# Kernel tuning notes

Measured on AMD Instinct MI355X. Metric: run time of the kernel, lower is better.

## Reference

```python
import jax, jax.numpy as jnp
import numpy as np

D_MODEL = 1024
NUM_HEADS = 16
DEPTH = D_MODEL // NUM_HEADS


def setup_inputs() -> dict:
    key = jax.random.key(0)
    ks = jax.random.split(key, 11)
    B, S = 2, 2048
    s = 1.0 / np.sqrt(D_MODEL)
    return {
        "q": jax.random.normal(ks[0], (B, S, D_MODEL), jnp.float32),
        "k": jax.random.normal(ks[1], (B, S, D_MODEL), jnp.float32),
        "v": jax.random.normal(ks[2], (B, S, D_MODEL), jnp.float32),
        "wq": jax.random.normal(ks[3], (D_MODEL, D_MODEL), jnp.float32) * s,
        "bq": jax.random.normal(ks[4], (D_MODEL,), jnp.float32) * s,
        "wk": jax.random.normal(ks[5], (D_MODEL, D_MODEL), jnp.float32) * s,
        "bk": jax.random.normal(ks[6], (D_MODEL,), jnp.float32) * s,
        "wv": jax.random.normal(ks[7], (D_MODEL, D_MODEL), jnp.float32) * s,
        "bv": jax.random.normal(ks[8], (D_MODEL,), jnp.float32) * s,
        "wo": jax.random.normal(ks[9], (D_MODEL, D_MODEL), jnp.float32) * s,
        "bo": jax.random.normal(ks[10], (D_MODEL,), jnp.float32) * s,
    }


def _split_heads(x, B):
    # [B, S, D] -> [B, H, S, depth]
    return x.reshape(B, -1, NUM_HEADS, DEPTH).transpose(0, 2, 1, 3)


def reference(q, k, v, wq, bq, wk, bk, wv, bv, wo, bo):
    B, S, _ = q.shape
    # torch Linear: y = x @ W.T + b
    qh = _split_heads(q @ wq.T + bq, B)
    kh = _split_heads(k @ wk.T + bk, B)
    vh = _split_heads(v @ wv.T + bv, B)
    scale = jnp.sqrt(jnp.asarray(DEPTH, jnp.float32))
    scores = jnp.einsum("bhqd,bhkd->bhqk", qh, kh) / scale  # [B,H,S,S]
    attn = jax.nn.softmax(scores, axis=-1)
    out = jnp.einsum("bhqk,bhkd->bhqd", attn, vh)
    out = out.transpose(0, 2, 1, 3).reshape(B, S, D_MODEL)
    return out @ wo.T + bo
```

## Files before the change

### kernel.cpp

```cpp
#include <hip/hip_runtime.h>
#include <hip/hip_bf16.h>
#include <math.h>

#define D_MODEL 1024
#define NUM_HEADS 16
#define DEPTH 64
#define BATCH 2
#define SEQ 2048
#define N_TOK (BATCH * SEQ)

typedef short bf16x8 __attribute__((ext_vector_type(8)));
typedef _Float16 f16x8 __attribute__((ext_vector_type(8)));
typedef float f32x4  __attribute__((ext_vector_type(4)));
typedef unsigned short u16x8 __attribute__((ext_vector_type(8)));
typedef unsigned short u16x4 __attribute__((ext_vector_type(4)));
typedef unsigned int u32x4 __attribute__((ext_vector_type(4)));

__device__ __forceinline__ unsigned short f2b(float x) {
    return __builtin_bit_cast(unsigned short, __float2bfloat16(x));
}
__device__ __forceinline__ float b2f(unsigned short h) {
    return __builtin_bit_cast(float, (unsigned int)h << 16);
}
__device__ __forceinline__ unsigned short f2h(float x) {
    return __builtin_bit_cast(unsigned short, (_Float16)x);
}

__device__ __forceinline__ void pl32_swap(unsigned int& x, unsigned int& y) {
    auto r = __builtin_amdgcn_permlane32_swap(x, y, false, false);
    x = (unsigned int)r[0]; y = (unsigned int)r[1];
}
__device__ __forceinline__ void pl16_swap(unsigned int& x, unsigned int& y) {
    auto r = __builtin_amdgcn_permlane16_swap(x, y, false, false);
    x = (unsigned int)r[0]; y = (unsigned int)r[1];
}

__global__ __launch_bounds__(256) void prep_weights(
    const float* __restrict__ s0, const float* __restrict__ s1,
    const float* __restrict__ s2, const float* __restrict__ s3,
    unsigned short* __restrict__ f0, unsigned short* __restrict__ f1,
    unsigned short* __restrict__ f2,
    unsigned short* __restrict__ h3, unsigned short* __restrict__ l3,
    int n8)
{
    const int i = blockIdx.x * 256 + threadIdx.x;
    if (i >= n8) return;
    const int which = blockIdx.y;
    const float* src = (which == 0) ? s0 : (which == 1) ? s1 : (which == 2) ? s2 : s3;
    const float4 a0 = ((const float4*)src)[2 * i];
    const float4 a1 = ((const float4*)src)[2 * i + 1];
    const float xs[8] = {a0.x, a0.y, a0.z, a0.w, a1.x, a1.y, a1.z, a1.w};
    if (which < 3) {
        unsigned short* dst = (which == 0) ? f0 : (which == 1) ? f1 : f2;
        u16x8 o;
        #pragma unroll
        for (int e = 0; e < 8; ++e) o[e] = f2h(xs[e]);
        *(u16x8*)&dst[(size_t)i * 8] = o;
    } else {
        u16x8 h8, l8;
        #pragma unroll
        for (int e = 0; e < 8; ++e) {
            const unsigned short h = f2b(xs[e]);
            h8[e] = h;
            l8[e] = f2b(xs[e] - b2f(h));
        }
        *(u16x8*)&h3[(size_t)i * 8] = h8;
        *(u16x8*)&l3[(size_t)i * 8] = l8;
    }
}

__global__ __launch_bounds__(256, 3) void qkv_gemm(
    const float* __restrict__ Aq, const float* __restrict__ Ak,
    const float* __restrict__ Av,
    const unsigned short* __restrict__ Wq, const unsigned short* __restrict__ Wk,
    const unsigned short* __restrict__ Wv,
    const float* __restrict__ bq, const float* __restrict__ bk,
    const float* __restrict__ bv,
    void* __restrict__ Yq, void* __restrict__ Yk, void* __restrict__ Yvp)
{
    __shared__ unsigned short sA[128][64];
    __shared__ unsigned short sB[2][128][64];

    const int flat = (blockIdx.z * 32 + blockIdx.y) * 8 + blockIdx.x;
    const int swz  = (flat & 7) * 96 + (flat >> 3);
    const int bx = swz & 7;
    const int by = (swz >> 3) & 31;
    const int bz = swz >> 8;

    const float* Af = (bz == 0) ? Aq : (bz == 1) ? Ak : Av;
    const unsigned short* Bf = (bz == 0) ? Wq : (bz == 1) ? Wk : Wv;
    const float* bias = (bz == 0) ? bq : (bz == 1) ? bk : bv;
    const float scale = (bz == 0) ? 0.125f : 1.0f;
    const int mode = (bz == 2) ? 2 : 1;
    void* Yv = (bz == 0) ? Yq : (bz == 1) ? Yk : Yvp;

    const int tid  = threadIdx.x;
    const int wave = tid >> 6;
    const int lane = tid & 63;
    const int quad = lane >> 4;
    const int l16  = lane & 15;
    const int wm   = wave >> 1;
    const int wn   = wave & 1;

    const int j0 = bx * 128;
    const int i0 = by * 128;

    const int sc  = tid & 7;
    const int r32 = tid >> 3;

    f32x4 acc[4][4] = {};

    float4 fq[4][2];

    auto loadA = [&](int s) {
        const int k0 = s * 64;
        #pragma unroll
        for (int p = 0; p < 4; ++p) {
            const int row = p * 32 + r32;
            const int cg = (sc ^ (row & 7)) * 8;
            const float* srcp = &Af[(size_t)(i0 + row) * 1024 + k0 + cg];
            fq[p][0] = *(const float4*)srcp;
            fq[p][1] = *(const float4*)(srcp + 4);
        }
    };
    auto writeA = [&]() {
        #pragma unroll
        for (int p = 0; p < 4; ++p) {
            const int row = p * 32 + r32;
            const float xs[8] = {fq[p][0].x, fq[p][0].y, fq[p][0].z, fq[p][0].w,
                                 fq[p][1].x, fq[p][1].y, fq[p][1].z, fq[p][1].w};
            u16x8 o;
            #pragma unroll
            for (int e = 0; e < 8; ++e) o[e] = f2h(xs[e]);
            *(u16x8*)&sA[row][sc * 8] = o;
        }
    };
    auto stageB = [&](int buf, int s) {
        const int k0 = s * 64;
        #pragma unroll
        for (int p = 0; p < 4; ++p) {
            const int row = p * 32 + r32;
            const int cg = (sc ^ (row & 7)) * 8;
            __builtin_amdgcn_global_load_lds(
                (const __attribute__((address_space(1))) unsigned int*)
                    &Bf[(size_t)(j0 + row) * 1024 + k0 + cg],
                (__attribute__((address_space(3))) unsigned int*)&sB[buf][row][sc * 8],
                16, 0, 0);
        }
    };

    loadA(0);
    stageB(0, 0);
    writeA();
    __asm__ volatile("s_waitcnt vmcnt(0)" ::: "memory");
    __syncthreads();

    int cur = 0;
    for (int s = 0; s < 16; ++s) {
        if (s + 1 < 16) { loadA(s + 1); stageB(cur ^ 1, s + 1); }

        #pragma unroll
        for (int ks = 0; ks < 2; ++ks) {
            f16x8 a[4], b[4];
            #pragma unroll
            for (int mt = 0; mt < 4; ++mt) {
                const int row = wm * 64 + mt * 16 + l16;
                const int c = (((ks * 4 + quad) ^ (row & 7))) * 8;
                a[mt] = *(const f16x8*)&sA[row][c];
            }
            #pragma unroll
            for (int nt = 0; nt < 4; ++nt) {
                const int row = wn * 64 + nt * 16 + l16;
                const int c = (((ks * 4 + quad) ^ (row & 7))) * 8;
                b[nt] = *(const f16x8*)&sB[cur][row][c];
            }
            #pragma unroll
            for (int mt = 0; mt < 4; ++mt)
                #pragma unroll
                for (int nt = 0; nt < 4; ++nt)
                    acc[mt][nt] = __builtin_amdgcn_mfma_f32_16x16x32_f16(a[mt], b[nt], acc[mt][nt], 0, 0, 0);
        }

        __syncthreads();
        if (s + 1 < 16) {
            writeA();
            __asm__ volatile("s_waitcnt vmcnt(0)" ::: "memory");
        }
        __syncthreads();
        cur ^= 1;
    }

    float bvv[4];
    #pragma unroll
    for (int nt = 0; nt < 4; ++nt)
        bvv[nt] = bias[j0 + wn * 64 + nt * 16 + l16];

    #pragma unroll
    for (int mt = 0; mt < 4; ++mt) {
        const int ibase = i0 + wm * 64 + mt * 16 + quad * 4;
        #pragma unroll
        for (int nt = 0; nt < 4; ++nt) {
            const int j = j0 + wn * 64 + nt * 16 + l16;
            const int h = j >> 6, d = j & 63;
            if (mode == 1) {
                __hip_bfloat16* Y = (__hip_bfloat16*)Yv;
                #pragma unroll
                for (int r = 0; r < 4; ++r) {
                    const int i = ibase + r;
                    const int b = i >> 11, ss = i & (SEQ - 1);
                    Y[(((size_t)(b * NUM_HEADS + h) * SEQ) + ss) * DEPTH + d] =
                        __float2bfloat16((acc[mt][nt][r] + bvv[nt]) * scale);
                }
            } else {
                unsigned short* Y = (unsigned short*)Yv;
                const int b = ibase >> 11;
                u16x4 pack;
                #pragma unroll
                for (int r = 0; r < 4; ++r)
                    pack[r] = f2b((acc[mt][nt][r] + bvv[nt]) * scale);
                *(u16x4*)&Y[(((size_t)(b * NUM_HEADS + h) * DEPTH) + d) * SEQ
                            + (ibase & (SEQ - 1))] = pack;
            }
        }
    }
}

__global__ __launch_bounds__(512, 2) void gemm_bf16x3(
    const unsigned short* __restrict__ Ahi,
    const unsigned short* __restrict__ Alo,
    const unsigned short* __restrict__ Bhi,
    const unsigned short* __restrict__ Blo,
    const float* __restrict__ bias,
    float* __restrict__ Y,
    float scale)
{
    __shared__ unsigned short sAh[128][64];
    __shared__ unsigned short sAl[128][64];
    __shared__ unsigned short sBh[128][64];
    __shared__ unsigned short sBl[128][64];

    const int tid  = threadIdx.x;
    const int wave = tid >> 6;
    const int lane = tid & 63;
    const int quad = lane >> 4;
    const int l16  = lane & 15;
    const int wm   = wave >> 1;
    const int wn   = wave & 1;

    const int j0 = blockIdx.x * 128;
    const int i0 = blockIdx.y * 128;

    const int sc  = tid & 7;
    const int r64 = tid >> 3;

    u16x8 preH[4], preL[4];

    #pragma unroll
    for (int p = 0; p < 4; ++p) {
        const int row256 = p * 64 + r64;
        const bool isA = row256 < 128;
        const int row = isA ? row256 : row256 - 128;
        const unsigned short* srcH = isA ? Ahi : Bhi;
        const unsigned short* srcL = isA ? Alo : Blo;
        const int grow = (isA ? i0 : j0) + row;
        const int cg = (sc ^ (row & 7)) * 8;
        const size_t go = (size_t)grow * 1024 + cg;
        preH[p] = *(const u16x8*)&srcH[go];
        preL[p] = *(const u16x8*)&srcL[go];
    }

    f32x4 acc[2][4] = {};

    for (int s = 0; s < 16; ++s) {
        __syncthreads();

        #pragma unroll
        for (int p = 0; p < 4; ++p) {
            const int row256 = p * 64 + r64;
            const bool isA = row256 < 128;
            const int row = isA ? row256 : row256 - 128;
            unsigned short (*dh)[64] = isA ? sAh : sBh;
            unsigned short (*dl)[64] = isA ? sAl : sBl;
            *(u16x8*)&dh[row][sc * 8] = preH[p];
            *(u16x8*)&dl[row][sc * 8] = preL[p];
        }
        __syncthreads();

        if (s + 1 < 16) {
            const int k0 = (s + 1) * 64;
            #pragma unroll
            for (int p = 0; p < 4; ++p) {
                const int row256 = p * 64 + r64;
                const bool isA = row256 < 128;
                const int row = isA ? row256 : row256 - 128;
                const unsigned short* srcH = isA ? Ahi : Bhi;
                const unsigned short* srcL = isA ? Alo : Blo;
                const int grow = (isA ? i0 : j0) + row;
                const int cg = (sc ^ (row & 7)) * 8;
                const size_t go = (size_t)grow * 1024 + k0 + cg;
                preH[p] = *(const u16x8*)&srcH[go];
                preL[p] = *(const u16x8*)&srcL[go];
            }
        }

        #pragma unroll
        for (int ks = 0; ks < 2; ++ks) {
            bf16x8 ah[2], al[2], bh[4], bl[4];
            #pragma unroll
            for (int mt = 0; mt < 2; ++mt) {
                const int row = wm * 32 + mt * 16 + l16;
                const int c = (((ks * 4 + quad) ^ (row & 7))) * 8;
                ah[mt] = *(const bf16x8*)&sAh[row][c];
                al[mt] = *(const bf16x8*)&sAl[row][c];
            }
            #pragma unroll
            for (int nt = 0; nt < 4; ++nt) {
                const int row = wn * 64 + nt * 16 + l16;
                const int c = (((ks * 4 + quad) ^ (row & 7))) * 8;
                bh[nt] = *(const bf16x8*)&sBh[row][c];
                bl[nt] = *(const bf16x8*)&sBl[row][c];
            }
            #pragma unroll
            for (int mt = 0; mt < 2; ++mt)
                #pragma unroll
                for (int nt = 0; nt < 4; ++nt) {
                    acc[mt][nt] = __builtin_amdgcn_mfma_f32_16x16x32_bf16(ah[mt], bh[nt], acc[mt][nt], 0, 0, 0);
                    acc[mt][nt] = __builtin_amdgcn_mfma_f32_16x16x32_bf16(ah[mt], bl[nt], acc[mt][nt], 0, 0, 0);
                    acc[mt][nt] = __builtin_amdgcn_mfma_f32_16x16x32_bf16(al[mt], bh[nt], acc[mt][nt], 0, 0, 0);
                }
        }
    }

    float bv[4];
    #pragma unroll
    for (int nt = 0; nt < 4; ++nt)
        bv[nt] = bias[j0 + wn * 64 + nt * 16 + l16];

    #pragma unroll
    for (int mt = 0; mt < 2; ++mt) {
        const int ibase = i0 + wm * 32 + mt * 16 + quad * 4;
        #pragma unroll
        for (int nt = 0; nt < 4; ++nt) {
            const int j = j0 + wn * 64 + nt * 16 + l16;
            #pragma unroll
            for (int r = 0; r < 4; ++r)
                Y[(size_t)(ibase + r) * 1024 + j] = (acc[mt][nt][r] + bv[nt]) * scale;
        }
    }
}

__global__ __launch_bounds__(256) void flash_attn_mfma(
    const __hip_bfloat16* __restrict__ Qg,
    const __hip_bfloat16* __restrict__ Kg,
    const __hip_bfloat16* __restrict__ Vg,
    unsigned short* __restrict__ OHi,
    unsigned short* __restrict__ OLo)
{
    __shared__ unsigned short Ks[64][72];
    __shared__ unsigned short Vt[64][72];

    const int tid  = threadIdx.x;
    const int wave = tid >> 6;
    const int lane = tid & 63;
    const int quad = lane >> 4;
    const int l16  = lane & 15;

    const int bh = blockIdx.x >> 5;
    const int q0 = (blockIdx.x & 31) * 64;

    const unsigned short* Qu = (const unsigned short*)Qg + (size_t)bh * SEQ * DEPTH;
    const unsigned short* Ku = (const unsigned short*)Kg + (size_t)bh * SEQ * DEPTH;
    const unsigned short* Vu = (const unsigned short*)Vg + (size_t)bh * DEPTH * SEQ;

    const int qrow = q0 + wave * 16 + l16;
    bf16x8 qf[2];
    qf[0] = *(const bf16x8*)&Qu[(size_t)qrow * DEPTH + quad * 8];
    qf[1] = *(const bf16x8*)&Qu[(size_t)qrow * DEPTH + 32 + quad * 8];

    bf16x8 ones;
    #pragma unroll
    for (int e = 0; e < 8; ++e) ones[e] = (short)0x3F80;

    f32x4 o_acc[4] = {};
    f32x4 l_acc = {0.f, 0.f, 0.f, 0.f};

    const int srow = tid >> 3;
    const int sc8  = (tid & 7) * 8;
    u16x8 kpre[2], vpre[2];
    #pragma unroll
    for (int it = 0; it < 2; ++it) {
        const int row = it * 32 + srow;
        kpre[it] = *(const u16x8*)&Ku[(size_t)row * DEPTH + sc8];
        vpre[it] = *(const u16x8*)&Vu[(size_t)row * SEQ + sc8];
    }

    for (int t = 0; t < 32; ++t) {
        __syncthreads();

        #pragma unroll
        for (int it = 0; it < 2; ++it) {
            const int row = it * 32 + srow;
            *(u16x8*)&Ks[row][sc8] = kpre[it];
            *(u16x8*)&Vt[row][sc8] = vpre[it];
        }
        __syncthreads();

        if (t + 1 < 32) {
            const int k0 = (t + 1) * 64;
            #pragma unroll
            for (int it = 0; it < 2; ++it) {
                const int row = it * 32 + srow;
                kpre[it] = *(const u16x8*)&Ku[(size_t)(k0 + row) * DEPTH + sc8];
                vpre[it] = *(const u16x8*)&Vu[(size_t)row * SEQ + k0 + sc8];
            }
        }

        f32x4 s[4];
        #pragma unroll
        for (int nt = 0; nt < 4; ++nt) {
            s[nt] = f32x4{0.f, 0.f, 0.f, 0.f};
            bf16x8 kf0 = *(const bf16x8*)&Ks[nt * 16 + l16][quad * 8];
            s[nt] = __builtin_amdgcn_mfma_f32_16x16x32_bf16(kf0, qf[0], s[nt], 0, 0, 0);
            bf16x8 kf1 = *(const bf16x8*)&Ks[nt * 16 + l16][32 + quad * 8];
            s[nt] = __builtin_amdgcn_mfma_f32_16x16x32_bf16(kf1, qf[1], s[nt], 0, 0, 0);
        }

        unsigned int Wp[4][2];
        #pragma unroll
        for (int nt = 0; nt < 4; ++nt) {
            #pragma unroll
            for (int b = 0; b < 2; ++b) {
                const unsigned int lo = f2b(__expf(s[nt][2 * b]));
                const unsigned int hi = f2b(__expf(s[nt][2 * b + 1]));
                Wp[nt][b] = lo | (hi << 16);
            }
        }

        unsigned int pw[8];
        #pragma unroll
        for (int b = 0; b < 2; ++b) {
            unsigned int x = Wp[0][b], y = Wp[1][b];
            pl32_swap(x, y);
            pl16_swap(x, y);
            pw[b] = x; pw[2 + b] = y;
            x = Wp[2][b]; y = Wp[3][b];
            pl32_swap(x, y);
            pl16_swap(x, y);
            pw[4 + b] = x; pw[6 + b] = y;
        }
        bf16x8 pf[2];
        {
            u32x4 t0, t1;
            #pragma unroll
            for (int j = 0; j < 4; ++j) { t0[j] = pw[j]; t1[j] = pw[4 + j]; }
            pf[0] = __builtin_bit_cast(bf16x8, t0);
            pf[1] = __builtin_bit_cast(bf16x8, t1);
        }

        #pragma unroll
        for (int nt = 0; nt < 4; ++nt) {
            bf16x8 vf0 = *(const bf16x8*)&Vt[nt * 16 + l16][quad * 8];
            o_acc[nt] = __builtin_amdgcn_mfma_f32_16x16x32_bf16(pf[0], vf0, o_acc[nt], 0, 0, 0);
            bf16x8 vf1 = *(const bf16x8*)&Vt[nt * 16 + l16][32 + quad * 8];
            o_acc[nt] = __builtin_amdgcn_mfma_f32_16x16x32_bf16(pf[1], vf1, o_acc[nt], 0, 0, 0);
        }
        l_acc = __builtin_amdgcn_mfma_f32_16x16x32_bf16(pf[0], ones, l_acc, 0, 0, 0);
        l_acc = __builtin_amdgcn_mfma_f32_16x16x32_bf16(pf[1], ones, l_acc, 0, 0, 0);
    }

    const int b = bh / NUM_HEADS;
    const int h = bh % NUM_HEADS;
    #pragma unroll
    for (int r = 0; r < 4; ++r) {
        const float inv = 1.f / l_acc[r];
        const int row = q0 + wave * 16 + quad * 4 + r;
        #pragma unroll
        for (int nt = 0; nt < 4; ++nt) {
            const float o = o_acc[nt][r] * inv;
            const size_t idx = ((size_t)(b * SEQ + row)) * D_MODEL + h * DEPTH + nt * 16 + l16;
            const unsigned short hbits = f2b(o);
            OHi[idx] = hbits;
            OLo[idx] = f2b(o - b2f(hbits));
        }
    }
}

extern "C" void kernel_launch(void* const* d_in, const int* in_sizes, int n_in,
                              void* d_out, int out_size, void* d_ws, size_t ws_size,
                              hipStream_t stream) {
    const float* q  = (const float*)d_in[0];
    const float* k  = (const float*)d_in[1];
    const float* v  = (const float*)d_in[2];
    const float* wq = (const float*)d_in[3];
    const float* bq = (const float*)d_in[4];
    const float* wk = (const float*)d_in[5];
    const float* bk = (const float*)d_in[6];
    const float* wv = (const float*)d_in[7];
    const float* bv = (const float*)d_in[8];
    const float* wo = (const float*)d_in[9];
    const float* bo = (const float*)d_in[10];
    float* out = (float*)d_out;

    char* ws = (char*)d_ws;
    const size_t MB = 1024 * 1024;
    unsigned short* AoHi = (unsigned short*)(ws);
    unsigned short* AoLo = (unsigned short*)(ws + 8 * MB);
    unsigned short* WqF  = (unsigned short*)(ws + 16 * MB);
    unsigned short* WkF  = (unsigned short*)(ws + 18 * MB);
    unsigned short* WvF  = (unsigned short*)(ws + 20 * MB);
    unsigned short* WoH  = (unsigned short*)(ws + 22 * MB);
    unsigned short* WoL  = (unsigned short*)(ws + 24 * MB);
    __hip_bfloat16* Qh   = (__hip_bfloat16*)(ws + 26 * MB);
    __hip_bfloat16* Kh   = (__hip_bfloat16*)(ws + 34 * MB);
    __hip_bfloat16* Vh   = (__hip_bfloat16*)(ws + 42 * MB);

    const int nW8 = D_MODEL * D_MODEL / 8;
    dim3 sb(256);

    prep_weights<<<dim3(nW8 / 256, 4), sb, 0, stream>>>(
        wq, wk, wv, wo, WqF, WkF, WvF, WoH, WoL, nW8);

    dim3 fblk(256);
    dim3 fgrid(D_MODEL / 128, N_TOK / 128, 3);
    qkv_gemm<<<fgrid, fblk, 0, stream>>>(
        q, k, v, WqF, WkF, WvF, bq, bk, bv, Qh, Kh, (void*)Vh);

    dim3 ablk(256);
    dim3 agrid(BATCH * NUM_HEADS * (SEQ / 64));
    flash_attn_mfma<<<agrid, ablk, 0, stream>>>(Qh, Kh, Vh, AoHi, AoLo);

    dim3 oblk(512);
    dim3 ogrid(D_MODEL / 128, N_TOK / 128);
    gemm_bf16x3<<<ogrid, oblk, 0, stream>>>(AoHi, AoLo, WoH, WoL, bo, out, 1.0f);
}
```

Measured before the change: 248.2 us.

## Process two query tiles per attention block to reuse K/V tiles

Each flash-attention block now handles 128 query rows instead of 64: every wave computes two 16-row query groups against the same shared-memory K and V tiles. This halves the number of blocks and the K/V global loads and LDS staging per query row. It also adds a block-index swizzle so that consecutive blocks land on different heads, plus a launch-bounds occupancy hint. The cost is more registers per thread for the doubled accumulators and only 512 blocks, which may hurt occupancy or load balance across the CUs.

```diff
diff --git a/kernel.cpp b/kernel.cpp
--- a/kernel.cpp
+++ b/kernel.cpp
@@ -349,7 +349,7 @@
     }
 }
 
-__global__ __launch_bounds__(256) void flash_attn_mfma(
+__global__ __launch_bounds__(256, 2) void flash_attn_mfma(
     const __hip_bfloat16* __restrict__ Qg,
     const __hip_bfloat16* __restrict__ Kg,
     const __hip_bfloat16* __restrict__ Vg,
@@ -365,24 +365,30 @@
     const int quad = lane >> 4;
     const int l16  = lane & 15;
 
-    const int bh = blockIdx.x >> 5;
-    const int q0 = (blockIdx.x & 31) * 64;
+    const int flat = blockIdx.x;
+    const int swz  = (flat & 7) * 64 + (flat >> 3);
+    const int bh = swz >> 4;
+    const int q0 = (swz & 15) * 128;
 
     const unsigned short* Qu = (const unsigned short*)Qg + (size_t)bh * SEQ * DEPTH;
     const unsigned short* Ku = (const unsigned short*)Kg + (size_t)bh * SEQ * DEPTH;
     const unsigned short* Vu = (const unsigned short*)Vg + (size_t)bh * DEPTH * SEQ;
 
-    const int qrow = q0 + wave * 16 + l16;
-    bf16x8 qf[2];
-    qf[0] = *(const bf16x8*)&Qu[(size_t)qrow * DEPTH + quad * 8];
-    qf[1] = *(const bf16x8*)&Qu[(size_t)qrow * DEPTH + 32 + quad * 8];
+    const int qrowA = q0 + wave * 16 + l16;
+    const int qrowB = qrowA + 64;
+    bf16x8 qfA[2], qfB[2];
+    qfA[0] = *(const bf16x8*)&Qu[(size_t)qrowA * DEPTH + quad * 8];
+    qfA[1] = *(const bf16x8*)&Qu[(size_t)qrowA * DEPTH + 32 + quad * 8];
+    qfB[0] = *(const bf16x8*)&Qu[(size_t)qrowB * DEPTH + quad * 8];
+    qfB[1] = *(const bf16x8*)&Qu[(size_t)qrowB * DEPTH + 32 + quad * 8];
 
     bf16x8 ones;
     #pragma unroll
     for (int e = 0; e < 8; ++e) ones[e] = (short)0x3F80;
 
-    f32x4 o_acc[4] = {};
-    f32x4 l_acc = {0.f, 0.f, 0.f, 0.f};
+    f32x4 o_accA[4] = {}, o_accB[4] = {};
+    f32x4 l_accA = {0.f, 0.f, 0.f, 0.f};
+    f32x4 l_accB = {0.f, 0.f, 0.f, 0.f};
 
     const int srow = tid >> 3;
     const int sc8  = (tid & 7) * 8;
@@ -394,37 +400,7 @@
         vpre[it] = *(const u16x8*)&Vu[(size_t)row * SEQ + sc8];
     }
 
-    for (int t = 0; t < 32; ++t) {
-        __syncthreads();
-
-        #pragma unroll
-        for (int it = 0; it < 2; ++it) {
-            const int row = it * 32 + srow;
-            *(u16x8*)&Ks[row][sc8] = kpre[it];
-            *(u16x8*)&Vt[row][sc8] = vpre[it];
-        }
-        __syncthreads();
-
-        if (t + 1 < 32) {
-            const int k0 = (t + 1) * 64;
-            #pragma unroll
-            for (int it = 0; it < 2; ++it) {
-                const int row = it * 32 + srow;
-                kpre[it] = *(const u16x8*)&Ku[(size_t)(k0 + row) * DEPTH + sc8];
-                vpre[it] = *(const u16x8*)&Vu[(size_t)row * SEQ + k0 + sc8];
-            }
-        }
-
-        f32x4 s[4];
-        #pragma unroll
-        for (int nt = 0; nt < 4; ++nt) {
-            s[nt] = f32x4{0.f, 0.f, 0.f, 0.f};
-            bf16x8 kf0 = *(const bf16x8*)&Ks[nt * 16 + l16][quad * 8];
-            s[nt] = __builtin_amdgcn_mfma_f32_16x16x32_bf16(kf0, qf[0], s[nt], 0, 0, 0);
-            bf16x8 kf1 = *(const bf16x8*)&Ks[nt * 16 + l16][32 + quad * 8];
-            s[nt] = __builtin_amdgcn_mfma_f32_16x16x32_bf16(kf1, qf[1], s[nt], 0, 0, 0);
-        }
-
+    auto make_pf = [&](const f32x4 s[4], bf16x8 pf[2]) {
         unsigned int Wp[4][2];
         #pragma unroll
         for (int nt = 0; nt < 4; ++nt) {
@@ -435,7 +411,6 @@
                 Wp[nt][b] = lo | (hi << 16);
             }
         }
-
         unsigned int pw[8];
         #pragma unroll
         for (int b = 0; b < 2; ++b) {
@@ -448,39 +423,90 @@
             pl16_swap(x, y);
             pw[4 + b] = x; pw[6 + b] = y;
         }
-        bf16x8 pf[2];
-        {
-            u32x4 t0, t1;
-            #pragma unroll
-            for (int j = 0; j < 4; ++j) { t0[j] = pw[j]; t1[j] = pw[4 + j]; }
-            pf[0] = __builtin_bit_cast(bf16x8, t0);
-            pf[1] = __builtin_bit_cast(bf16x8, t1);
-        }
+        u32x4 t0, t1;
+        #pragma unroll
+        for (int j = 0; j < 4; ++j) { t0[j] = pw[j]; t1[j] = pw[4 + j]; }
+        pf[0] = __builtin_bit_cast(bf16x8, t0);
+        pf[1] = __builtin_bit_cast(bf16x8, t1);
+    };
+
+    for (int t = 0; t < 32; ++t) {
+        __syncthreads();
+
+        #pragma unroll
+        for (int it = 0; it < 2; ++it) {
+            const int row = it * 32 + srow;
+            *(u16x8*)&Ks[row][sc8] = kpre[it];
+            *(u16x8*)&Vt[row][sc8] = vpre[it];
+        }
+        __syncthreads();
+
+        if (t + 1 < 32) {
+            const int k0 = (t + 1) * 64;
+            #pragma unroll
+            for (int it = 0; it < 2; ++it) {
+                const int row = it * 32 + srow;
+                kpre[it] = *(const u16x8*)&Ku[(size_t)(k0 + row) * DEPTH + sc8];
+                vpre[it] = *(const u16x8*)&Vu[(size_t)row * SEQ + k0 + sc8];
+            }
+        }
+
+        f32x4 sA[4], sB[4];
+        #pragma unroll
+        for (int nt = 0; nt < 4; ++nt) {
+            sA[nt] = f32x4{0.f, 0.f, 0.f, 0.f};
+            sB[nt] = f32x4{0.f, 0.f, 0.f, 0.f};
+            bf16x8 kf0 = *(const bf16x8*)&Ks[nt * 16 + l16][quad * 8];
+            sA[nt] = __builtin_amdgcn_mfma_f32_16x16x32_bf16(kf0, qfA[0], sA[nt], 0, 0, 0);
+            sB[nt] = __builtin_amdgcn_mfma_f32_16x16x32_bf16(kf0, qfB[0], sB[nt], 0, 0, 0);
+            bf16x8 kf1 = *(const bf16x8*)&Ks[nt * 16 + l16][32 + quad * 8];
+            sA[nt] = __builtin_amdgcn_mfma_f32_16x16x32_bf16(kf1, qfA[1], sA[nt], 0, 0, 0);
+            sB[nt] = __builtin_amdgcn_mfma_f32_16x16x32_bf16(kf1, qfB[1], sB[nt], 0, 0, 0);
+        }
+
+        bf16x8 pfA[2], pfB[2];
+        make_pf(sA, pfA);
+        make_pf(sB, pfB);
 
         #pragma unroll
         for (int nt = 0; nt < 4; ++nt) {
             bf16x8 vf0 = *(const bf16x8*)&Vt[nt * 16 + l16][quad * 8];
-            o_acc[nt] = __builtin_amdgcn_mfma_f32_16x16x32_bf16(pf[0], vf0, o_acc[nt], 0, 0, 0);
+            o_accA[nt] = __builtin_amdgcn_mfma_f32_16x16x32_bf16(pfA[0], vf0, o_accA[nt], 0, 0, 0);
+            o_accB[nt] = __builtin_amdgcn_mfma_f32_16x16x32_bf16(pfB[0], vf0, o_accB[nt], 0, 0, 0);
             bf16x8 vf1 = *(const bf16x8*)&Vt[nt * 16 + l16][32 + quad * 8];
-            o_acc[nt] = __builtin_amdgcn_mfma_f32_16x16x32_bf16(pf[1], vf1, o_acc[nt], 0, 0, 0);
-        }
-        l_acc = __builtin_amdgcn_mfma_f32_16x16x32_bf16(pf[0], ones, l_acc, 0, 0, 0);
-        l_acc = __builtin_amdgcn_mfma_f32_16x16x32_bf16(pf[1], ones, l_acc, 0, 0, 0);
+            o_accA[nt] = __builtin_amdgcn_mfma_f32_16x16x32_bf16(pfA[1], vf1, o_accA[nt], 0, 0, 0);
+            o_accB[nt] = __builtin_amdgcn_mfma_f32_16x16x32_bf16(pfB[1], vf1, o_accB[nt], 0, 0, 0);
+        }
+        l_accA = __builtin_amdgcn_mfma_f32_16x16x32_bf16(pfA[0], ones, l_accA, 0, 0, 0);
+        l_accA = __builtin_amdgcn_mfma_f32_16x16x32_bf16(pfA[1], ones, l_accA, 0, 0, 0);
+        l_accB = __builtin_amdgcn_mfma_f32_16x16x32_bf16(pfB[0], ones, l_accB, 0, 0, 0);
+        l_accB = __builtin_amdgcn_mfma_f32_16x16x32_bf16(pfB[1], ones, l_accB, 0, 0, 0);
     }
 
     const int b = bh / NUM_HEADS;
     const int h = bh % NUM_HEADS;
     #pragma unroll
     for (int r = 0; r < 4; ++r) {
-        const float inv = 1.f / l_acc[r];
-        const int row = q0 + wave * 16 + quad * 4 + r;
+        const float invA = 1.f / l_accA[r];
+        const float invB = 1.f / l_accB[r];
+        const int rowA = q0 + wave * 16 + quad * 4 + r;
+        const int rowB = rowA + 64;
         #pragma unroll
         for (int nt = 0; nt < 4; ++nt) {
-            const float o = o_acc[nt][r] * inv;
-            const size_t idx = ((size_t)(b * SEQ + row)) * D_MODEL + h * DEPTH + nt * 16 + l16;
-            const unsigned short hbits = f2b(o);
-            OHi[idx] = hbits;
-            OLo[idx] = f2b(o - b2f(hbits));
+            {
+                const float o = o_accA[nt][r] * invA;
+                const size_t idx = ((size_t)(b * SEQ + rowA)) * D_MODEL + h * DEPTH + nt * 16 + l16;
+                const unsigned short hbits = f2b(o);
+                OHi[idx] = hbits;
+                OLo[idx] = f2b(o - b2f(hbits));
+            }
+            {
+                const float o = o_accB[nt][r] * invB;
+                const size_t idx = ((size_t)(b * SEQ + rowB)) * D_MODEL + h * DEPTH + nt * 16 + l16;
+                const unsigned short hbits = f2b(o);
+                OHi[idx] = hbits;
+                OLo[idx] = f2b(o - b2f(hbits));
+            }
         }
     }
 }
@@ -526,7 +552,7 @@
         q, k, v, WqF, WkF, WvF, bq, bk, bv, Qh, Kh, (void*)Vh);
 
     dim3 ablk(256);
-    dim3 agrid(BATCH * NUM_HEADS * (SEQ / 64));
+    dim3 agrid(BATCH * NUM_HEADS * (SEQ / 128));
     flash_attn_mfma<<<agrid, ablk, 0, stream>>>(Qh, Kh, Vh, AoHi, AoLo);
 
     dim3 oblk(512);
```

After: 240.1 us. 1.03x faster.
